# Kernel tuning notes

Hardware: AMD Instinct MI355X
Metric: run time of the kernel (lower is better)

Reference implementation:

```python
import jax, jax.numpy as jnp
import numpy as np

N_NODES = 100000
N_EDGES = 1600000
IN_CH = 128
OUT_CH = 32
HEADS = 2
NEG_SLOPE = 0.2  # GATv2Conv default negative_slope


def setup_inputs() -> dict:
    key = jax.random.key(0)
    ks = jax.random.split(key, 6)
    x = jax.random.normal(ks[0], (N_NODES, IN_CH), dtype=jnp.float32)
    edge_index = jax.random.randint(ks[1], (2, N_EDGES), 0, N_NODES, dtype=jnp.int64)
    s_in = 1.0 / np.sqrt(IN_CH)
    Wl = jax.random.normal(ks[2], (IN_CH, HEADS * OUT_CH), dtype=jnp.float32) * s_in  # lin_l weight
    Wr = jax.random.normal(ks[3], (IN_CH, HEADS * OUT_CH), dtype=jnp.float32) * s_in  # lin_r weight
    bl = jnp.zeros((HEADS * OUT_CH,), dtype=jnp.float32)
    br = jnp.zeros((HEADS * OUT_CH,), dtype=jnp.float32)
    att = jax.random.normal(ks[4], (HEADS, OUT_CH), dtype=jnp.float32) * (1.0 / np.sqrt(OUT_CH))
    bias = jnp.zeros((OUT_CH,), dtype=jnp.float32)  # output bias (concat=False -> size out_channels)
    return {"x": x, "Wl": Wl, "bl": bl, "Wr": Wr, "br": br, "att": att, "bias": bias,
            "edge_index": edge_index}


def _gatv2_layer(x, Wl, bl, Wr, br, att, bias, edge_index):
    N = x.shape[0]
    H, C = att.shape
    # add self loops (GATv2Conv default add_self_loops=True)
    loops = jnp.arange(N, dtype=edge_index.dtype)
    src = jnp.concatenate([edge_index[0], loops])  # [E+N] message sources j
    dst = jnp.concatenate([edge_index[1], loops])  # [E+N] message targets i
    # per-node linear transforms (share_weights=False)
    xl = (x @ Wl + bl).reshape(N, H, C)
    xr = (x @ Wr + br).reshape(N, H, C)
    # GATv2 dynamic attention: a^T LeakyReLU(xl[j] + xr[i])
    h = xl[src] + xr[dst]                                   # [E, H, C]
    e = jnp.einsum('ehc,hc->eh', jax.nn.leaky_relu(h, NEG_SLOPE), att)  # [E, H]
    # segment softmax over incoming edges of each target node
    m = jax.ops.segment_max(e, dst, num_segments=N)         # [N, H]
    a = jnp.exp(e - m[dst])
    denom = jax.ops.segment_sum(a, dst, num_segments=N)     # [N, H]
    alpha = a / (denom[dst] + 1e-16)                        # [E, H]
    # weighted scatter-add of source messages
    out = jax.ops.segment_sum(alpha[:, :, None] * xl[src], dst, num_segments=N)  # [N, H, C]
    out = out.mean(axis=1) + bias                           # concat=False -> head mean
    return jax.nn.silu(out)                                 # activation='silu'


def reference(x, Wl, bl, Wr, br, att, bias, edge_index):
    return _gatv2_layer(x, Wl, bl, Wr, br, att, bias, edge_index)
```

## Files before the change

kernel.cpp:

```cpp
#include <hip/hip_runtime.h>
#include <math.h>

#define BSH 9
#define BMASK ((1 << BSH) - 1)
#define CAP 12288
#define ACH 2048

typedef unsigned int uint;
typedef __attribute__((ext_vector_type(8))) short bf16x8;
typedef __attribute__((ext_vector_type(4))) float f32x4;
typedef __attribute__((ext_vector_type(2))) float f32x2;

static __device__ __forceinline__ unsigned short f2bf(float f) {
    uint u = __float_as_uint(f);
    return (unsigned short)((u + 0x7fffu + ((u >> 16) & 1u)) >> 16);
}

static __device__ __forceinline__ bf16x8 pack8(float4 a, float4 b) {
    uint p0, p1, p2, p3;
    asm("v_cvt_pk_bf16_f32 %0, %1, %2" : "=v"(p0) : "v"(a.x), "v"(a.y));
    asm("v_cvt_pk_bf16_f32 %0, %1, %2" : "=v"(p1) : "v"(a.z), "v"(a.w));
    asm("v_cvt_pk_bf16_f32 %0, %1, %2" : "=v"(p2) : "v"(b.x), "v"(b.y));
    asm("v_cvt_pk_bf16_f32 %0, %1, %2" : "=v"(p3) : "v"(b.z), "v"(b.w));
    uint4 u = make_uint4(p0, p1, p2, p3);
    return *(bf16x8*)&u;
}

static __device__ __forceinline__ f32x2 dec2(uint u) {
    f32x2 r;
    r.x = __uint_as_float(u << 16);
    r.y = __uint_as_float(u & 0xffff0000u);
    return r;
}

static __device__ __forceinline__ f32x2 abs2(f32x2 h) {
    f32x2 r;
    r.x = __uint_as_float(__float_as_uint(h.x) & 0x7fffffffu);
    r.y = __uint_as_float(__float_as_uint(h.y) & 0x7fffffffu);
    return r;
}

static __device__ __forceinline__ float qsum(float p) {
    p += __uint_as_float(__builtin_amdgcn_mov_dpp(__float_as_uint(p), 0xB1, 0xF, 0xF, true));
    p += __uint_as_float(__builtin_amdgcn_mov_dpp(__float_as_uint(p), 0x4E, 0xF, 0xF, true));
    return p;
}

static __device__ __forceinline__ void gemm_body(char* sB,
        const float* __restrict__ x,
        const float* __restrict__ Wl, const float* __restrict__ bl,
        const float* __restrict__ Wr, const float* __restrict__ br,
        unsigned short* __restrict__ xlh, float* __restrict__ xr, int N, int bid)
{
    const int t = threadIdx.x;
    const int base = bid * 128;

#pragma unroll
    for (int s = 0; s < 8; ++s) {
        int tau = s * 256 + t;
        int m  = tau >> 10;
        int k2 = (tau >> 4) & 63;
        int n4 = tau & 15;
        const float4* Wp = (const float4*)(m ? Wr : Wl);
        float4 a = Wp[(2 * k2) * 16 + n4];
        float4 b = Wp[(2 * k2 + 1) * 16 + n4];
        const float* af = (const float*)&a;
        const float* bf = (const float*)&b;
#pragma unroll
        for (int j = 0; j < 4; ++j) {
            int n = m * 64 + n4 * 4 + j;
            uint u = (uint)f2bf(af[j]) | ((uint)f2bf(bf[j]) << 16);
            *(uint*)(sB + n * 256 + ((k2 * 4) ^ ((n & 15) << 4))) = u;
        }
    }
    __syncthreads();

    const int w = t >> 6;
    const int lo = t & 15;
    const int hi = (t & 63) >> 4;
    int row0 = base + w * 32 + lo;
    int row1 = row0 + 16;
    const float4* x40 = (const float4*)x + (size_t)(row0 < N ? row0 : N - 1) * 32;
    const float4* x41 = (const float4*)x + (size_t)(row1 < N ? row1 : N - 1) * 32;

    f32x4 acc[2][8];
#pragma unroll
    for (int f = 0; f < 2; ++f)
#pragma unroll
        for (int j = 0; j < 8; ++j)
            acc[f][j] = (f32x4){0.f, 0.f, 0.f, 0.f};

#pragma unroll
    for (int ks = 0; ks < 4; ++ks) {
        int kb = ks * 64 + hi * 16;
        int f4 = ks * 8 + hi * 2;
        bf16x8 av[2], bv[8];
        av[0] = pack8(x40[f4], x40[f4 + 1]);
        av[1] = pack8(x41[f4], x41[f4 + 1]);
#pragma unroll
        for (int j = 0; j < 8; ++j) {
            int nn = j * 16 + lo;
            bv[j] = *(const bf16x8*)(sB + nn * 256 + (kb ^ ((nn & 15) << 4)));
        }
#pragma unroll
        for (int f = 0; f < 2; ++f)
#pragma unroll
            for (int j = 0; j < 8; ++j)
                acc[f][j] = __builtin_amdgcn_mfma_f32_16x16x32_bf16(av[f], bv[j], acc[f][j], 0, 0, 0);
    }

#pragma unroll
    for (int f = 0; f < 2; ++f) {
        int rbase = base + w * 32 + f * 16 + hi * 4;
#pragma unroll
        for (int j = 0; j < 8; ++j) {
            int nn = j * 16 + lo;
            float bvv = (j < 4) ? bl[nn] : br[nn - 64];
            float vv[4] = {acc[f][j][0] + bvv, acc[f][j][1] + bvv,
                           acc[f][j][2] + bvv, acc[f][j][3] + bvv};
            if (j < 4) {
#pragma unroll
                for (int q = 0; q < 4; ++q)
                    if (rbase + q < N) xlh[(size_t)(rbase + q) * 64 + nn] = f2bf(vv[q]);
            } else {
#pragma unroll
                for (int q = 0; q < 4; ++q)
                    if (rbase + q < N) xr[(size_t)(rbase + q) * 64 + (nn - 64)] = vv[q];
            }
        }
    }
}

static __device__ __forceinline__ void scatA_body(char* smem,
        const int* __restrict__ ei, int* __restrict__ bcur,
        unsigned* __restrict__ pairs, int E, int T, int NB, int bid)
{
    int* h = (int*)smem;
    int* basem = h + 256;
    int b0 = bid * ACH;
    int cnt = min(ACH, T - b0);
    h[threadIdx.x] = 0;
    __syncthreads();
    for (int i = threadIdx.x; i < cnt; i += 256) {
        int t = b0 + i;
        int d = (t < E) ? ei[E + t] : (t - E);
        atomicAdd(&h[d >> BSH], 1);
    }
    __syncthreads();
    if (threadIdx.x < NB) {
        int c = h[threadIdx.x];
        basem[threadIdx.x] = c ? (threadIdx.x * CAP + atomicAdd(&bcur[threadIdx.x], c)) : 0;
    }
    __syncthreads();
    h[threadIdx.x] = 0;
    __syncthreads();
    for (int i = threadIdx.x; i < cnt; i += 256) {
        int t = b0 + i;
        int s, d;
        if (t < E) { s = ei[t]; d = ei[E + t]; } else { s = t - E; d = s; }
        int b = d >> BSH;
        int idx = atomicAdd(&h[b], 1);
        pairs[basem[b] + idx] = ((unsigned)s << BSH) | (unsigned)(d & BMASK);
    }
}

__global__ __launch_bounds__(256, 4) void k_gs(const float* __restrict__ x,
        const float* __restrict__ Wl, const float* __restrict__ bl,
        const float* __restrict__ Wr, const float* __restrict__ br,
        unsigned short* __restrict__ xlh, float* __restrict__ xr, int N,
        const int* __restrict__ ei, int* __restrict__ bcur,
        unsigned* __restrict__ pairs, int E, int T, int NB, int GB)
{
    extern __shared__ char smem[];
    if ((int)blockIdx.x < GB)
        gemm_body(smem, x, Wl, bl, Wr, br, xlh, xr, N, blockIdx.x);
    else
        scatA_body(smem, ei, bcur, pairs, E, T, NB, blockIdx.x - GB);
}

__global__ __launch_bounds__(512) void k_scatB(const unsigned* __restrict__ pairs,
                                               const int* __restrict__ bcur,
                                               int* __restrict__ src_s, int2* __restrict__ rowrng, int N) {
    __shared__ int cnt[512];
    __shared__ int sm[512];
    __shared__ int lofs[512];
    int b = blockIdx.x;
    int beg = b * CAP, end = beg + bcur[b];
    int nbase = b << BSH;
    cnt[threadIdx.x] = 0;
    __syncthreads();
    for (int i = beg + threadIdx.x; i < end; i += 512)
        atomicAdd(&cnt[pairs[i] & BMASK], 1);
    __syncthreads();
    int v = cnt[threadIdx.x];
    sm[threadIdx.x] = v;
    __syncthreads();
    int acc = v;
    for (int off = 1; off < 512; off <<= 1) {
        int t = (threadIdx.x >= off) ? sm[threadIdx.x - off] : 0;
        __syncthreads();
        acc += t;
        sm[threadIdx.x] = acc;
        __syncthreads();
    }
    int excl = acc - v;
    lofs[threadIdx.x] = excl;
    int n = nbase + threadIdx.x;
    if (n < N) rowrng[n] = make_int2(beg + excl, beg + excl + v);
    cnt[threadIdx.x] = 0;
    __syncthreads();
    for (int i = beg + threadIdx.x; i < end; i += 512) {
        unsigned p = pairs[i];
        int dl = p & BMASK;
        int idx = atomicAdd(&cnt[dl], 1);
        src_s[beg + lofs[dl] + idx] = p >> BSH;
    }
}

__global__ __launch_bounds__(256) void k_fused(const int2* __restrict__ rowrng,
        const int* __restrict__ src_s, const unsigned short* __restrict__ xlh,
        const float* __restrict__ xr, const float* __restrict__ att,
        const float* __restrict__ bias, float* __restrict__ out, int N)
{
    int n = blockIdx.x * 32 + (threadIdx.x >> 3);
    int j = threadIdx.x & 7;
    if (n >= N) return;
    const uint4* xl4 = (const uint4*)xlh + j;
    f32x2 xr2[4], a06[4], a04[4];
    {
        float4 a = ((const float4*)xr)[(size_t)n * 16 + j * 2];
        float4 b = ((const float4*)xr)[(size_t)n * 16 + j * 2 + 1];
        xr2[0] = (f32x2){a.x, a.y}; xr2[1] = (f32x2){a.z, a.w};
        xr2[2] = (f32x2){b.x, b.y}; xr2[3] = (f32x2){b.z, b.w};
        float4 c = ((const float4*)att)[j * 2];
        float4 d = ((const float4*)att)[j * 2 + 1];
        a06[0] = (f32x2){0.6f * c.x, 0.6f * c.y}; a06[1] = (f32x2){0.6f * c.z, 0.6f * c.w};
        a06[2] = (f32x2){0.6f * d.x, 0.6f * d.y}; a06[3] = (f32x2){0.6f * d.z, 0.6f * d.w};
        a04[0] = (f32x2){0.4f * c.x, 0.4f * c.y}; a04[1] = (f32x2){0.4f * c.z, 0.4f * c.w};
        a04[2] = (f32x2){0.4f * d.x, 0.4f * d.y}; a04[3] = (f32x2){0.4f * d.z, 0.4f * d.w};
    }
    int2 rr = rowrng[n];
    float ssum = 0.f;
    f32x2 acc2[4] = {(f32x2){0.f,0.f}, (f32x2){0.f,0.f}, (f32x2){0.f,0.f}, (f32x2){0.f,0.f}};

#define EDGE_BODY(u)                                                      \
    {                                                                     \
        f32x2 v0 = dec2((u).x), v1 = dec2((u).y), v2 = dec2((u).z), v3 = dec2((u).w); \
        f32x2 h0 = v0 + xr2[0], h1 = v1 + xr2[1], h2 = v2 + xr2[2], h3 = v3 + xr2[3]; \
        f32x2 pa = h0 * a06[0]; pa += h1 * a06[1]; pa += h2 * a06[2]; pa += h3 * a06[3]; \
        pa += abs2(h0) * a04[0]; pa += abs2(h1) * a04[1];                 \
        pa += abs2(h2) * a04[2]; pa += abs2(h3) * a04[3];                 \
        float p = pa.x + pa.y;                                            \
        p = qsum(p);                                                      \
        float wq = __expf(p);                                             \
        ssum += wq;                                                       \
        f32x2 ws = (f32x2){wq, wq};                                       \
        acc2[0] += ws * v0; acc2[1] += ws * v1;                           \
        acc2[2] += ws * v2; acc2[3] += ws * v3;                           \
    }

    int i = rr.x;
    for (; i + 8 <= rr.y; i += 8) {
        uint4 u[8];
#pragma unroll
        for (int q = 0; q < 8; ++q)
            u[q] = xl4[((uint)src_s[i + q] << 3)];
#pragma unroll
        for (int q = 0; q < 8; ++q)
            EDGE_BODY(u[q]);
    }
    if (i + 4 <= rr.y) {
        uint4 u[4];
#pragma unroll
        for (int q = 0; q < 4; ++q)
            u[q] = xl4[((uint)src_s[i + q] << 3)];
#pragma unroll
        for (int q = 0; q < 4; ++q)
            EDGE_BODY(u[q]);
        i += 4;
    }
    for (; i < rr.y; ++i) {
        uint4 u0 = xl4[((uint)src_s[i] << 3)];
        EDGE_BODY(u0);
    }
#undef EDGE_BODY

    float inv = 1.f / ssum;
    float o[8];
#pragma unroll
    for (int q = 0; q < 4; ++q) {
        float vx = acc2[q].x * inv, vy = acc2[q].y * inv;
        o[2 * q]     = (vx + __shfl_xor(vx, 4)) * 0.5f;
        o[2 * q + 1] = (vy + __shfl_xor(vy, 4)) * 0.5f;
    }
    if (j < 4) {
        float4 b0 = ((const float4*)bias)[j * 2];
        float4 b1 = ((const float4*)bias)[j * 2 + 1];
        float4 r0, r1;
        r0.x = o[0] + b0.x; r0.y = o[1] + b0.y; r0.z = o[2] + b0.z; r0.w = o[3] + b0.w;
        r1.x = o[4] + b1.x; r1.y = o[5] + b1.y; r1.z = o[6] + b1.z; r1.w = o[7] + b1.w;
        r0.x = r0.x / (1.f + __expf(-r0.x));
        r0.y = r0.y / (1.f + __expf(-r0.y));
        r0.z = r0.z / (1.f + __expf(-r0.z));
        r0.w = r0.w / (1.f + __expf(-r0.w));
        r1.x = r1.x / (1.f + __expf(-r1.x));
        r1.y = r1.y / (1.f + __expf(-r1.y));
        r1.z = r1.z / (1.f + __expf(-r1.z));
        r1.w = r1.w / (1.f + __expf(-r1.w));
        ((float4*)out)[(size_t)n * 8 + j * 2] = r0;
        ((float4*)out)[(size_t)n * 8 + j * 2 + 1] = r1;
    }
}

extern "C" void kernel_launch(void* const* d_in, const int* in_sizes, int n_in,
                              void* d_out, int out_size, void* d_ws, size_t ws_size,
                              hipStream_t stream) {
    const float* x    = (const float*)d_in[0];
    const float* Wl   = (const float*)d_in[1];
    const float* bl   = (const float*)d_in[2];
    const float* Wr   = (const float*)d_in[3];
    const float* br   = (const float*)d_in[4];
    const float* att  = (const float*)d_in[5];
    const float* bias = (const float*)d_in[6];
    const int*   ei   = (const int*)d_in[7];
    float* out = (float*)d_out;

    const int N = in_sizes[0] / 128;
    const int E = in_sizes[7] / 2;
    const int T = E + N;
    const int NB = (N + (1 << BSH) - 1) >> BSH;

    char* p = (char*)d_ws;
    auto take = [&](size_t bytes) {
        char* r = p;
        p += (bytes + 255) & ~(size_t)255;
        return r;
    };
    unsigned short* xlh = (unsigned short*)take((size_t)N * 64 * 2);
    float*    xr     = (float*)take((size_t)N * 64 * 4);
    unsigned* pairs  = (unsigned*)take((size_t)NB * CAP * 4);
    int*      src_s  = (int*)take((size_t)NB * CAP * 4);
    int2*     rowrng = (int2*)take((size_t)N * 8);
    int*      bcur   = (int*)take((size_t)NB * 4);

    const int GB = (N + 127) / 128;
    const int SB = (T + ACH - 1) / ACH;
    hipMemsetAsync(bcur, 0, (size_t)NB * 4, stream);
    k_gs   <<<GB + SB,       256, 32768, stream>>>(x, Wl, bl, Wr, br, xlh, xr, N,
                                                   ei, bcur, pairs, E, T, NB, GB);
    k_scatB<<<NB,            512, 0, stream>>>(pairs, bcur, src_s, rowrng, N);
    k_fused<<<(N + 31) / 32, 256, 0, stream>>>(rowrng, src_s, xlh, xr, att, bias, out, N);
}
```

Before: 103.9 us.

## Precompute bf16 transposed weights once and read B operand from global memory

Adds a small prep kernel that converts Wl and Wr to a transposed bf16 matrix once per call. The GEMM blocks then load B fragments directly from global memory (L2/L1 cached) instead of having every block convert weights into a 32KB LDS buffer and synchronise. Dropping the dynamic LDS allocation lets more blocks fit per CU and removes per-block redundant conversion work. The cost is an extra kernel launch and uncoalesced-ish global reads of B fragments per wave.

Measured after the change: 121.9 us. +17.3%, slower.

```diff
diff --git a/kernel.cpp b/kernel.cpp
--- a/kernel.cpp
+++ b/kernel.cpp
@@ -46,35 +46,41 @@
     return p;
 }
 
-static __device__ __forceinline__ void gemm_body(char* sB,
-        const float* __restrict__ x,
-        const float* __restrict__ Wl, const float* __restrict__ bl,
-        const float* __restrict__ Wr, const float* __restrict__ br,
+__global__ __launch_bounds__(256) void k_prep(const float* __restrict__ Wl,
+                                              const float* __restrict__ Wr,
+                                              unsigned short* __restrict__ Wt) {
+    __shared__ unsigned short s[16][130];
+    int b = blockIdx.x;
+    int t = threadIdx.x;
+#pragma unroll
+    for (int i = 0; i < 8; ++i) {
+        int idx = i * 256 + t;
+        int kl = idx >> 7;
+        int n  = idx & 127;
+        int k  = b * 16 + kl;
+        float v = (n < 64) ? Wl[k * 64 + n] : Wr[k * 64 + (n - 64)];
+        s[kl][n] = f2bf(v);
+    }
+    __syncthreads();
+#pragma unroll
+    for (int i = 0; i < 2; ++i) {
+        int idx = i * 256 + t;
+        int n  = idx >> 2;
+        int kg = idx & 3;
+        ushort4 v;
+        v.x = s[kg * 4 + 0][n]; v.y = s[kg * 4 + 1][n];
+        v.z = s[kg * 4 + 2][n]; v.w = s[kg * 4 + 3][n];
+        *(ushort4*)(Wt + n * 128 + b * 16 + kg * 4) = v;
+    }
+}
+
+static __device__ __forceinline__ void gemm_body(
+        const float* __restrict__ x, const unsigned short* __restrict__ Wt,
+        const float* __restrict__ bl, const float* __restrict__ br,
         unsigned short* __restrict__ xlh, float* __restrict__ xr, int N, int bid)
 {
     const int t = threadIdx.x;
     const int base = bid * 128;
-
-#pragma unroll
-    for (int s = 0; s < 8; ++s) {
-        int tau = s * 256 + t;
-        int m  = tau >> 10;
-        int k2 = (tau >> 4) & 63;
-        int n4 = tau & 15;
-        const float4* Wp = (const float4*)(m ? Wr : Wl);
-        float4 a = Wp[(2 * k2) * 16 + n4];
-        float4 b = Wp[(2 * k2 + 1) * 16 + n4];
-        const float* af = (const float*)&a;
-        const float* bf = (const float*)&b;
-#pragma unroll
-        for (int j = 0; j < 4; ++j) {
-            int n = m * 64 + n4 * 4 + j;
-            uint u = (uint)f2bf(af[j]) | ((uint)f2bf(bf[j]) << 16);
-            *(uint*)(sB + n * 256 + ((k2 * 4) ^ ((n & 15) << 4))) = u;
-        }
-    }
-    __syncthreads();
-
     const int w = t >> 6;
     const int lo = t & 15;
     const int hi = (t & 63) >> 4;
@@ -92,15 +98,15 @@
 
 #pragma unroll
     for (int ks = 0; ks < 4; ++ks) {
-        int kb = ks * 64 + hi * 16;
         int f4 = ks * 8 + hi * 2;
+        int kofs = ks * 32 + hi * 8;
         bf16x8 av[2], bv[8];
         av[0] = pack8(x40[f4], x40[f4 + 1]);
         av[1] = pack8(x41[f4], x41[f4 + 1]);
 #pragma unroll
         for (int j = 0; j < 8; ++j) {
             int nn = j * 16 + lo;
-            bv[j] = *(const bf16x8*)(sB + nn * 256 + (kb ^ ((nn & 15) << 4)));
+            bv[j] = *(const bf16x8*)(Wt + nn * 128 + kofs);
         }
 #pragma unroll
         for (int f = 0; f < 2; ++f)
@@ -131,12 +137,12 @@
     }
 }
 
-static __device__ __forceinline__ void scatA_body(char* smem,
+static __device__ __forceinline__ void scatA_body(
         const int* __restrict__ ei, int* __restrict__ bcur,
         unsigned* __restrict__ pairs, int E, int T, int NB, int bid)
 {
-    int* h = (int*)smem;
-    int* basem = h + 256;
+    __shared__ int h[256];
+    __shared__ int basem[256];
     int b0 = bid * ACH;
     int cnt = min(ACH, T - b0);
     h[threadIdx.x] = 0;
@@ -164,18 +170,17 @@
     }
 }
 
-__global__ __launch_bounds__(256, 4) void k_gs(const float* __restrict__ x,
-        const float* __restrict__ Wl, const float* __restrict__ bl,
-        const float* __restrict__ Wr, const float* __restrict__ br,
+__global__ __launch_bounds__(256) void k_gs(const float* __restrict__ x,
+        const unsigned short* __restrict__ Wt,
+        const float* __restrict__ bl, const float* __restrict__ br,
         unsigned short* __restrict__ xlh, float* __restrict__ xr, int N,
         const int* __restrict__ ei, int* __restrict__ bcur,
         unsigned* __restrict__ pairs, int E, int T, int NB, int GB)
 {
-    extern __shared__ char smem[];
     if ((int)blockIdx.x < GB)
-        gemm_body(smem, x, Wl, bl, Wr, br, xlh, xr, N, blockIdx.x);
+        gemm_body(x, Wt, bl, br, xlh, xr, N, blockIdx.x);
     else
-        scatA_body(smem, ei, bcur, pairs, E, T, NB, blockIdx.x - GB);
+        scatA_body(ei, bcur, pairs, E, T, NB, blockIdx.x - GB);
 }
 
 __global__ __launch_bounds__(512) void k_scatB(const unsigned* __restrict__ pairs,
@@ -342,12 +347,14 @@
     int*      src_s  = (int*)take((size_t)NB * CAP * 4);
     int2*     rowrng = (int2*)take((size_t)N * 8);
     int*      bcur   = (int*)take((size_t)NB * 4);
+    unsigned short* Wt = (unsigned short*)take((size_t)128 * 128 * 2);
 
     const int GB = (N + 127) / 128;
     const int SB = (T + ACH - 1) / ACH;
     hipMemsetAsync(bcur, 0, (size_t)NB * 4, stream);
-    k_gs   <<<GB + SB,       256, 32768, stream>>>(x, Wl, bl, Wr, br, xlh, xr, N,
-                                                   ei, bcur, pairs, E, T, NB, GB);
+    k_prep <<<8,             256, 0, stream>>>(Wl, Wr, Wt);
+    k_gs   <<<GB + SB,       256, 0, stream>>>(x, Wt, bl, br, xlh, xr, N,
+                                               ei, bcur, pairs, E, T, NB, GB);
     k_scatB<<<NB,            512, 0, stream>>>(pairs, bcur, src_s, rowrng, N);
     k_fused<<<(N + 31) / 32, 256, 0, stream>>>(rowrng, src_s, xlh, xr, att, bias, out, N);
 }
```
